# Performance work log

Measured on AMD Instinct MI355X. Metric: run time of the kernel, lower is better.

The kernel has to match this reference:

```python
import jax, jax.numpy as jnp
import numpy as np

# Static problem dims (match input_specs)
B, N, C, H, W = 1, 3, 128, 256, 256
HEADS = 4
# _compute_dynamic_scales(256,256) with max_attention_size=4096:
# min_scale = max(2, int(sqrt(65536/4096))) = 4 -> scales [4,8,16], sorted desc:
SCALES = [16, 8, 4]


def setup_inputs() -> dict:
    key = jax.random.key(0)
    ks = jax.random.split(key, 8)
    S = len(SCALES)
    std = 0.05  # small init to keep logits in a sane range
    return {
        "query": jax.random.normal(ks[0], (B, C, H, W), jnp.float32),
        "keys": jax.random.normal(ks[1], (B, N, C, H, W), jnp.float32),
        "values": jax.random.normal(ks[2], (B, N, C, H, W), jnp.float32),
        "wq": jax.random.normal(ks[3], (S, C, C), jnp.float32) * std,
        "bq": jnp.zeros((S, C), jnp.float32),
        "wk": jax.random.normal(ks[4], (S, C, C), jnp.float32) * std,
        "bk": jnp.zeros((S, C), jnp.float32),
        "wv": jax.random.normal(ks[5], (S, C, C), jnp.float32) * std,
        "bv": jnp.zeros((S, C), jnp.float32),
        "fusion_w": jax.random.normal(ks[6], (C, 3 * C), jnp.float32) * std,
        "fusion_b": jnp.zeros((C,), jnp.float32),
        "out_w": jax.random.normal(ks[7], (C, C), jnp.float32) * std,
        "out_b": jnp.zeros((C,), jnp.float32),
    }


def _pool(x, s):
    """Average pool by integer factor s over the last two dims (adaptive_avg_pool2d
    with divisible sizes)."""
    *lead, c, h, w = x.shape
    return x.reshape(*lead, c, h // s, s, w // s, s).mean(axis=(-3, -1))


def _conv1x1(x, w, b):
    # x: [..., C_in, H, W], w: [C_out, C_in], b: [C_out]
    y = jnp.einsum('...chw,oc->...ohw', x, w)
    return y + b.reshape((1,) * (y.ndim - 3) + (-1, 1, 1))


def reference(query, keys, values, wq, bq, wk, bk, wv, bv,
              fusion_w, fusion_b, out_w, out_b):
    hd = C // HEADS
    outs = []
    for si, s in enumerate(SCALES):
        Hs, Ws = H // s, W // s
        L = Hs * Ws
        q_s = _pool(query, s)   # [B,C,Hs,Ws]
        k_s = _pool(keys, s)    # [B,N,C,Hs,Ws]
        v_s = _pool(values, s)  # [B,N,C,Hs,Ws]
        q = _conv1x1(q_s, wq[si], bq[si])
        k = _conv1x1(k_s, wk[si], bk[si])
        v = _conv1x1(v_s, wv[si], bv[si])
        q = q.reshape(B, HEADS, hd, L).transpose(0, 1, 3, 2)       # [B,h,L,d]
        k = k.reshape(B, N, HEADS, hd, L)                          # [B,N,h,d,M]
        v = v.reshape(B, N, HEADS, hd, L).transpose(0, 1, 2, 4, 3) # [B,N,h,M,d]
        scores = jnp.einsum('bhld,bnhdm->bnhlm', q, k) * (hd ** -0.5)
        attn = jax.nn.softmax(scores, axis=-1)                      # stable softmax
        out = jnp.einsum('bnhlm,bnhmd->bnhld', attn, v).mean(axis=1)  # mean over anchors
        out = out.transpose(0, 1, 3, 2).reshape(B, C, Hs, Ws)
        if s > 1:
            # F.interpolate bilinear, align_corners=False (half-pixel centers)
            out = jax.image.resize(out, (B, C, H, W), method='bilinear')
        outs.append(out)
    fused = jnp.concatenate(outs, axis=1)  # [B, 3C, H, W]
    y = _conv1x1(fused, fusion_w, fusion_b)
    return _conv1x1(y, out_w, out_b)
```

## Files before the change

### kernel.cpp

```cpp
#include <hip/hip_runtime.h>
#include <hip/hip_bf16.h>


typedef __attribute__((ext_vector_type(8))) short bf16x8;
typedef __attribute__((ext_vector_type(4))) float f32x4;

__device__ inline ushort rne_bf16(float x) {
  uint u = __float_as_uint(x);
  return (ushort)((u + 0x7fffu + ((u >> 16) & 1u)) >> 16);
}

__device__ inline uint pk2_bf16(float a, float b) {
  float2 f2; f2.x = a; f2.y = b;
  __hip_bfloat162 h = __float22bfloat162_rn(f2);
  union { __hip_bfloat162 h; uint u; } cvt; cvt.h = h;
  return cvt.u;
}

__global__ __launch_bounds__(256) void pool4_kernel(
    const float* __restrict__ query, const float* __restrict__ keys,
    const float* __restrict__ values, float* __restrict__ out)
{
  int idx = blockIdx.x * 256 + threadIdx.x;
  int x = idx & 63, y = (idx >> 6) & 63, mc = idx >> 12;
  int map = mc >> 7, c = mc & 127;
  const float* src;
  if (map == 0)      src = query  + (size_t)c * 65536;
  else if (map <= 3) src = keys   + (size_t)((map - 1) * 128 + c) * 65536;
  else               src = values + (size_t)((map - 4) * 128 + c) * 65536;
  src += (y * 4) * 256 + x * 4;
  float s = 0.f;
#pragma unroll
  for (int r = 0; r < 4; ++r) {
    float4 v = *(const float4*)(src + r * 256);
    s += v.x + v.y + v.z + v.w;
  }
  out[idx] = s * 0.0625f;
}

__global__ __launch_bounds__(256) void pool2_kernel(
    const float* __restrict__ in, float* __restrict__ out, int hw)
{
  int idx = blockIdx.x * 256 + threadIdx.x;
  int x = idx % hw; int y = (idx / hw) % hw; int mc = idx / (hw * hw);
  int w2 = hw * 2;
  const float* s = in + (size_t)mc * w2 * w2 + (2 * y) * w2 + 2 * x;
  float2 a = *(const float2*)s;
  float2 b = *(const float2*)(s + w2);
  out[idx] = (a.x + a.y + b.x + b.y) * 0.25f;
}

__global__ __launch_bounds__(256) void precomp_kernel(
    const float* __restrict__ fusion_w, const float* __restrict__ fusion_b,
    const float* __restrict__ out_w, const float* __restrict__ out_b,
    float* __restrict__ Wc, float* __restrict__ bc)
{
  int idx = blockIdx.x * 256 + threadIdx.x;
  if (idx < 128 * 384) {
    int o = idx / 384, k = idx % 384;
    float s = 0.f;
    for (int c = 0; c < 128; ++c)
      s = fmaf(out_w[o * 128 + c], fusion_w[c * 384 + k], s);
    Wc[idx] = s;
  } else if (idx < 128 * 384 + 128) {
    int o = idx - 128 * 384;
    float s = out_b[o];
    for (int c = 0; c < 128; ++c)
      s = fmaf(out_w[o * 128 + c], fusion_b[c], s);
    bc[o] = s;
  }
}

__global__ __launch_bounds__(256) void proj_kernel(
    const float* __restrict__ pooled,
    ushort* __restrict__ qb, ushort* __restrict__ kbb, ushort* __restrict__ vbb,
    const float* __restrict__ wq, const float* __restrict__ bq,
    const float* __restrict__ wk, const float* __restrict__ bk,
    const float* __restrict__ wv, const float* __restrict__ bv,
    int si, int L, float qscale)
{
  __shared__ float Wt[32][68];
  __shared__ float Xs[32][64];
  int map = blockIdx.z;
  int o0 = blockIdx.y * 64;
  int l0 = blockIdx.x * 64;
  const float* w; const float* b; float sc = 1.f;
  if (map == 0)      { w = wq + si * 16384; b = bq + si * 128; sc = qscale; }
  else if (map <= 3) { w = wk + si * 16384; b = bk + si * 128; }
  else               { w = wv + si * 16384; b = bv + si * 128; }
  const float* src = pooled + (size_t)map * 128 * L;
  int t = threadIdx.x;
  int og = t >> 4, lg = t & 15;
  float acc[4][4] = {};
  for (int c0 = 0; c0 < 128; c0 += 32) {
    __syncthreads();
    {
      int o = t >> 2, ci = (t & 3) * 8;
      const float* wp = w + (o0 + o) * 128 + c0 + ci;
      float4 a = *(const float4*)wp, d = *(const float4*)(wp + 4);
      Wt[ci + 0][o] = a.x; Wt[ci + 1][o] = a.y; Wt[ci + 2][o] = a.z; Wt[ci + 3][o] = a.w;
      Wt[ci + 4][o] = d.x; Wt[ci + 5][o] = d.y; Wt[ci + 6][o] = d.z; Wt[ci + 7][o] = d.w;
    }
    {
      int c = t >> 3, li = (t & 7) * 8;
      const float* xp = src + (size_t)(c0 + c) * L + l0 + li;
      float4 a = *(const float4*)xp, d = *(const float4*)(xp + 4);
      *(float4*)&Xs[c][li] = a; *(float4*)&Xs[c][li + 4] = d;
    }
    __syncthreads();
#pragma unroll 8
    for (int k = 0; k < 32; ++k) {
      float4 wv4 = *(const float4*)&Wt[k][4 * og];
      float4 xv4 = *(const float4*)&Xs[k][4 * lg];
      float wa[4] = {wv4.x, wv4.y, wv4.z, wv4.w};
      float xa[4] = {xv4.x, xv4.y, xv4.z, xv4.w};
#pragma unroll
      for (int r = 0; r < 4; ++r)
#pragma unroll
        for (int c = 0; c < 4; ++c)
          acc[r][c] = fmaf(wa[r], xa[c], acc[r][c]);
    }
  }
  float4 b4 = *(const float4*)&b[o0 + 4 * og];
  float ba[4] = {b4.x, b4.y, b4.z, b4.w};
  if (map < 4) {
    ushort* dst = (map == 0) ? qb : (kbb + (size_t)(map - 1) * L * 32 * 4);
    int o4 = o0 + 4 * og;
    size_t hbase = (size_t)(o4 >> 5) * L * 32 + (o4 & 31);
#pragma unroll
    for (int li = 0; li < 4; ++li) {
      ushort4 r;
      r.x = rne_bf16((acc[0][li] + ba[0]) * sc);
      r.y = rne_bf16((acc[1][li] + ba[1]) * sc);
      r.z = rne_bf16((acc[2][li] + ba[2]) * sc);
      r.w = rne_bf16((acc[3][li] + ba[3]) * sc);
      *(ushort4*)&dst[hbase + (size_t)(l0 + 4 * lg + li) * 32] = r;
    }
  } else {
    ushort* dst = vbb + (size_t)(map - 4) * 128 * L;
    int m = l0 + 4 * lg;
#pragma unroll
    for (int oi = 0; oi < 4; ++oi) {
      int o = o0 + 4 * og + oi;
      int h = o >> 5, d = o & 31;
      ushort4 r;
      r.x = rne_bf16(acc[oi][0] + ba[oi]);
      r.y = rne_bf16(acc[oi][1] + ba[oi]);
      r.z = rne_bf16(acc[oi][2] + ba[oi]);
      r.w = rne_bf16(acc[oi][3] + ba[oi]);
      size_t off = (size_t)h * 32 * L
                 + ((size_t)(m >> 5) * 2 + (d >> 4)) * 512
                 + (size_t)(d & 15) * 32 + ((m >> 3) & 3) * 8 + (m & 7);
      *(ushort4*)&dst[off] = r;
    }
  }
}

#define PSTR 72
__global__ __launch_bounds__(256, 4) void attn_mfma_kernel(
    const ushort* __restrict__ qb, const ushort* __restrict__ kb,
    const ushort* __restrict__ vb, float* __restrict__ onp,
    float* __restrict__ lsp, int L, int msplit)
{
  __shared__ __align__(16) ushort P[2][4][16][PSTR];
  int t = threadIdx.x;
  int wave = t >> 6, lane = t & 63;
  int col = lane & 15, quad = lane >> 4;
  int head = blockIdx.y;
  int anchor = blockIdx.z / msplit, mpart = blockIdx.z % msplit;
  int l = blockIdx.x * 64 + wave * 16;
  int mlen = L / msplit, mbase = mpart * mlen;
  int ntile = mlen >> 6;

  const ushort* qh = qb + (size_t)head * L * 32;
  const ushort* kh = kb + ((size_t)anchor * 4 + head) * L * 32;
  const ushort* vh = vb + ((size_t)anchor * 4 + head) * 32 * L;

  bf16x8 qf = *(const bf16x8*)(qh + (size_t)(l + col) * 32 + quad * 8);
  const ushort* kbase = kh + (size_t)mbase * 32 + col * 32 + quad * 8;
  const ushort* vbase = vh + (size_t)(mbase >> 5) * 1024 + col * 32 + quad * 8;

  f32x4 od0 = {0.f,0.f,0.f,0.f};
  f32x4 od1 = {0.f,0.f,0.f,0.f};
  f32x4 lsa = {0.f,0.f,0.f,0.f};
  const f32x4 z = {0.f,0.f,0.f,0.f};
  const bf16x8 ones = {16256,16256,16256,16256,16256,16256,16256,16256};

  ushort* Pa = &P[0][wave][0][0];
  ushort* Pb = &P[1][wave][0][0];

  auto expstore = [&](f32x4 a0, f32x4 a1, f32x4 a2, f32x4 a3, ushort* Pw) {
    float sv[4][4] = {{a0.x,a0.y,a0.z,a0.w},{a1.x,a1.y,a1.z,a1.w},
                      {a2.x,a2.y,a2.z,a2.w},{a3.x,a3.y,a3.z,a3.w}};
#pragma unroll
    for (int j = 0; j < 4; ++j) {
      uint u0 = pk2_bf16(__builtin_amdgcn_exp2f(sv[j][0]),
                         __builtin_amdgcn_exp2f(sv[j][1]));
      uint u1 = pk2_bf16(__builtin_amdgcn_exp2f(sv[j][2]),
                         __builtin_amdgcn_exp2f(sv[j][3]));
      uint2 dw; dw.x = u0; dw.y = u1;
      *(uint2*)&Pw[col * PSTR + 16 * j + quad * 4] = dw;
    }
  };

  bf16x8 k0 = *(const bf16x8*)(kbase);
  bf16x8 k1 = *(const bf16x8*)(kbase + 512);
  bf16x8 k2 = *(const bf16x8*)(kbase + 1024);
  bf16x8 k3 = *(const bf16x8*)(kbase + 1536);
  f32x4 s0 = __builtin_amdgcn_mfma_f32_16x16x32_bf16(k0, qf, z, 0, 0, 0);
  f32x4 s1 = __builtin_amdgcn_mfma_f32_16x16x32_bf16(k1, qf, z, 0, 0, 0);
  f32x4 s2 = __builtin_amdgcn_mfma_f32_16x16x32_bf16(k2, qf, z, 0, 0, 0);
  f32x4 s3 = __builtin_amdgcn_mfma_f32_16x16x32_bf16(k3, qf, z, 0, 0, 0);
  {
    const ushort* kp1 = kbase + ((ntile > 1) ? 64 * 32 : 0);
    k0 = *(const bf16x8*)(kp1);
    k1 = *(const bf16x8*)(kp1 + 512);
    k2 = *(const bf16x8*)(kp1 + 1024);
    k3 = *(const bf16x8*)(kp1 + 1536);
  }
  expstore(s0, s1, s2, s3, Pa);

  for (int i = 1; i < ntile; ++i) {
    const ushort* kpn = kbase + ((i + 1 < ntile) ? (i + 1) * 2048 : 0);
    bf16x8 n0 = *(const bf16x8*)(kpn);
    bf16x8 n1 = *(const bf16x8*)(kpn + 512);
    bf16x8 n2 = *(const bf16x8*)(kpn + 1024);
    bf16x8 n3 = *(const bf16x8*)(kpn + 1536);
    const ushort* vpn = vbase + (i - 1) * 2048;
    bf16x8 vA = *(const bf16x8*)(vpn);
    bf16x8 vB = *(const bf16x8*)(vpn + 1024);
    bf16x8 vC = *(const bf16x8*)(vpn + 512);
    bf16x8 vD = *(const bf16x8*)(vpn + 1536);
    bf16x8 p0 = *(const bf16x8*)(&Pa[col * PSTR + quad * 8]);
    bf16x8 p1 = *(const bf16x8*)(&Pa[col * PSTR + 32 + quad * 8]);
    f32x4 t0 = __builtin_amdgcn_mfma_f32_16x16x32_bf16(k0, qf, z, 0, 0, 0);
    f32x4 t1 = __builtin_amdgcn_mfma_f32_16x16x32_bf16(k1, qf, z, 0, 0, 0);
    f32x4 t2 = __builtin_amdgcn_mfma_f32_16x16x32_bf16(k2, qf, z, 0, 0, 0);
    f32x4 t3 = __builtin_amdgcn_mfma_f32_16x16x32_bf16(k3, qf, z, 0, 0, 0);
    lsa = __builtin_amdgcn_mfma_f32_16x16x32_bf16(p0, ones, lsa, 0, 0, 0);
    lsa = __builtin_amdgcn_mfma_f32_16x16x32_bf16(p1, ones, lsa, 0, 0, 0);
    od0 = __builtin_amdgcn_mfma_f32_16x16x32_bf16(p0, vA, od0, 0, 0, 0);
    od0 = __builtin_amdgcn_mfma_f32_16x16x32_bf16(p1, vB, od0, 0, 0, 0);
    od1 = __builtin_amdgcn_mfma_f32_16x16x32_bf16(p0, vC, od1, 0, 0, 0);
    od1 = __builtin_amdgcn_mfma_f32_16x16x32_bf16(p1, vD, od1, 0, 0, 0);
    expstore(t0, t1, t2, t3, Pb);
    k0 = n0; k1 = n1; k2 = n2; k3 = n3;
    ushort* tp = Pa; Pa = Pb; Pb = tp;
  }

  {
    const ushort* vpe = vbase + (ntile - 1) * 2048;
    bf16x8 vA = *(const bf16x8*)(vpe);
    bf16x8 vB = *(const bf16x8*)(vpe + 1024);
    bf16x8 vC = *(const bf16x8*)(vpe + 512);
    bf16x8 vD = *(const bf16x8*)(vpe + 1536);
    bf16x8 p0 = *(const bf16x8*)(&Pa[col * PSTR + quad * 8]);
    bf16x8 p1 = *(const bf16x8*)(&Pa[col * PSTR + 32 + quad * 8]);
    lsa = __builtin_amdgcn_mfma_f32_16x16x32_bf16(p0, ones, lsa, 0, 0, 0);
    lsa = __builtin_amdgcn_mfma_f32_16x16x32_bf16(p1, ones, lsa, 0, 0, 0);
    od0 = __builtin_amdgcn_mfma_f32_16x16x32_bf16(p0, vA, od0, 0, 0, 0);
    od0 = __builtin_amdgcn_mfma_f32_16x16x32_bf16(p1, vB, od0, 0, 0, 0);
    od1 = __builtin_amdgcn_mfma_f32_16x16x32_bf16(p0, vC, od1, 0, 0, 0);
    od1 = __builtin_amdgcn_mfma_f32_16x16x32_bf16(p1, vD, od1, 0, 0, 0);
  }

  float* on2 = onp + ((size_t)(mpart * 3 + anchor) * 128 + (size_t)(head * 32)) * L;
  float* ls2 = lsp + ((size_t)(mpart * 3 + anchor) * 4 + head) * L;
  if (col == 0)
    *(f32x4*)&ls2[l + quad * 4] = lsa;
  *(f32x4*)&on2[(size_t)col * L + l + quad * 4]        = od0;
  *(f32x4*)&on2[(size_t)(16 + col) * L + l + quad * 4] = od1;
}

__global__ __launch_bounds__(256) void norm_kernel(
    const float* __restrict__ on4,  const float* __restrict__ ls4,  float* __restrict__ a4,
    const float* __restrict__ on8,  const float* __restrict__ ls8,  float* __restrict__ a8,
    const float* __restrict__ on16, const float* __restrict__ ls16, float* __restrict__ a16)
{
  int i = blockIdx.x * 256 + threadIdx.x;
  const float* on; const float* ls; float* ax; int L; int ms;
  if (i < 131072)      { on = on4;  ls = ls4;  ax = a4;  L = 4096; ms = 2; }
  else if (i < 163840) { i -= 131072; on = on8;  ls = ls8;  ax = a8;  L = 1024; ms = 2; }
  else                 { i -= 163840; on = on16; ls = ls16; ax = a16; L = 256; ms = 4; }
  int e = i * 4;
  int c = e / L, l = e % L;
  int h = c >> 5;
  float ax0 = 0.f, ax1 = 0.f, ax2 = 0.f, ax3 = 0.f;
  for (int a = 0; a < 3; ++a) {
    float n0 = 0.f, n1 = 0.f, n2 = 0.f, n3 = 0.f;
    float d0 = 0.f, d1 = 0.f, d2 = 0.f, d3 = 0.f;
    for (int mp = 0; mp < ms; ++mp) {
      int g = mp * 3 + a;
      float4 o = *(const float4*)&on[((size_t)g * 128 + c) * L + l];
      float4 s = *(const float4*)&ls[((size_t)g * 4 + h) * L + l];
      n0 += o.x; n1 += o.y; n2 += o.z; n3 += o.w;
      d0 += s.x; d1 += s.y; d2 += s.z; d3 += s.w;
    }
    ax0 += n0 / d0; ax1 += n1 / d1; ax2 += n2 / d2; ax3 += n3 / d3;
  }
  const float third = 1.f / 3.f;
  float4 r = make_float4(ax0 * third, ax1 * third, ax2 * third, ax3 * third);
  *(float4*)&ax[e] = r;
}

__global__ __launch_bounds__(256) void ygemm_kernel(
    const float* __restrict__ a16, const float* __restrict__ a8,
    const float* __restrict__ a4, const float* __restrict__ Wc,
    float* __restrict__ y16, float* __restrict__ y8, float* __restrict__ y4)
{
  __shared__ float Wt[32][68];
  __shared__ float Xs[32][64];
  int bx = blockIdx.x;
  int o0 = blockIdx.y * 64;
  int sci; int lt; const float* src; float* dst; int L;
  if (bx < 4)       { sci = 0; lt = bx;      src = a16; dst = y16; L = 256; }
  else if (bx < 20) { sci = 1; lt = bx - 4;  src = a8;  dst = y8;  L = 1024; }
  else              { sci = 2; lt = bx - 20; src = a4;  dst = y4;  L = 4096; }
  int l0 = lt * 64;
  int coff = sci * 128;
  int t = threadIdx.x;
  int og = t >> 4, lg = t & 15;
  float acc[4][4] = {};
  for (int c0 = 0; c0 < 128; c0 += 32) {
    __syncthreads();
    {
      int o = t >> 2, ci = (t & 3) * 8;
      const float* wp = Wc + (o0 + o) * 384 + coff + c0 + ci;
      float4 a = *(const float4*)wp, d = *(const float4*)(wp + 4);
      Wt[ci + 0][o] = a.x; Wt[ci + 1][o] = a.y; Wt[ci + 2][o] = a.z; Wt[ci + 3][o] = a.w;
      Wt[ci + 4][o] = d.x; Wt[ci + 5][o] = d.y; Wt[ci + 6][o] = d.z; Wt[ci + 7][o] = d.w;
    }
    {
      int c = t >> 3, li = (t & 7) * 8;
      const float* xp = src + (size_t)(c0 + c) * L + l0 + li;
      float4 a = *(const float4*)xp, d = *(const float4*)(xp + 4);
      *(float4*)&Xs[c][li] = a; *(float4*)&Xs[c][li + 4] = d;
    }
    __syncthreads();
#pragma unroll 8
    for (int k = 0; k < 32; ++k) {
      float4 wv4 = *(const float4*)&Wt[k][4 * og];
      float4 xv4 = *(const float4*)&Xs[k][4 * lg];
      float wa[4] = {wv4.x, wv4.y, wv4.z, wv4.w};
      float xa[4] = {xv4.x, xv4.y, xv4.z, xv4.w};
#pragma unroll
      for (int r = 0; r < 4; ++r)
#pragma unroll
        for (int c = 0; c < 4; ++c)
          acc[r][c] = fmaf(wa[r], xa[c], acc[r][c]);
    }
  }
#pragma unroll
  for (int r = 0; r < 4; ++r) {
    float4 v = make_float4(acc[r][0], acc[r][1], acc[r][2], acc[r][3]);
    *(float4*)&dst[(size_t)(o0 + 4 * og + r) * L + l0 + 4 * lg] = v;
  }
}

__device__ inline void add_bilinear(const float* __restrict__ Yrow0,
                                    const float* __restrict__ Yrow1,
                                    int ssz, float sf, float fy,
                                    int px0, float* r)
{
#pragma unroll
  for (int j = 0; j < 4; ++j) {
    float sx = (px0 + j + 0.5f) * sf - 0.5f;
    int xi = (int)floorf(sx);
    float fx = sx - xi;
    int x0 = max(xi, 0), x1 = min(xi + 1, ssz - 1);
    float a0 = Yrow0[x0], a1 = Yrow0[x1];
    float b0 = Yrow1[x0], b1 = Yrow1[x1];
    float v0 = a0 + fx * (a1 - a0);
    float v1 = b0 + fx * (b1 - b0);
    r[j] += v0 + fy * (v1 - v0);
  }
}

__global__ __launch_bounds__(256) void upsample_kernel(
    const float* __restrict__ y16, const float* __restrict__ y8,
    const float* __restrict__ y4, const float* __restrict__ bc,
    float* __restrict__ outp)
{
  int idx = blockIdx.x * 256 + threadIdx.x;
  int x4 = idx & 63, py = (idx >> 6) & 255, o = idx >> 14;
  int px0 = x4 * 4;
  float b = bc[o];
  float r[4] = {b, b, b, b};
#pragma unroll
  for (int s = 0; s < 3; ++s) {
    const float* Y; int ssz; float sf;
    if (s == 0)      { Y = y16; ssz = 16; sf = 1.f / 16.f; }
    else if (s == 1) { Y = y8;  ssz = 32; sf = 1.f / 8.f; }
    else             { Y = y4;  ssz = 64; sf = 1.f / 4.f; }
    const float* Yo = Y + (size_t)o * ssz * ssz;
    float sy = (py + 0.5f) * sf - 0.5f;
    int yi = (int)floorf(sy);
    float fy = sy - yi;
    int yy0 = max(yi, 0), yy1 = min(yi + 1, ssz - 1);
    add_bilinear(Yo + yy0 * ssz, Yo + yy1 * ssz, ssz, sf, fy, px0, r);
  }
  float4 v = make_float4(r[0], r[1], r[2], r[3]);
  *(float4*)&outp[(size_t)o * 65536 + py * 256 + px0] = v;
}

extern "C" void kernel_launch(void* const* d_in, const int* in_sizes, int n_in,
                              void* d_out, int out_size, void* d_ws, size_t ws_size,
                              hipStream_t stream) {
  const float* query    = (const float*)d_in[0];
  const float* keys     = (const float*)d_in[1];
  const float* values   = (const float*)d_in[2];
  const float* wq       = (const float*)d_in[3];
  const float* bq       = (const float*)d_in[4];
  const float* wk       = (const float*)d_in[5];
  const float* bk       = (const float*)d_in[6];
  const float* wv       = (const float*)d_in[7];
  const float* bv       = (const float*)d_in[8];
  const float* fusion_w = (const float*)d_in[9];
  const float* fusion_b = (const float*)d_in[10];
  const float* out_w    = (const float*)d_in[11];
  const float* out_b    = (const float*)d_in[12];
  float* wsf  = (float*)d_ws;
  float* outp = (float*)d_out;

  const size_t P4   = 0;
  const size_t P8   = 3670016;
  const size_t P16  = 4587520;
  const size_t ONP4  = 0;
  const size_t LSP4  = 3145728;
  const size_t ONP8  = 3244032;
  const size_t LSP8  = 4030464;
  const size_t ONP16 = 4055040;
  const size_t LSP16 = 4448256;
  const size_t Y4   = 0;
  const size_t Y8   = 524288;
  const size_t Y16  = 655360;
  const size_t QB4  = 4816896;
  const size_t KB4  = 5079040;
  const size_t VB4  = 5865472;
  const size_t QB8  = 6651904;
  const size_t KB8  = 6717440;
  const size_t VB8  = 6914048;
  const size_t QB16 = 7110656;
  const size_t KB16 = 7127040;
  const size_t VB16 = 7176192;
  const size_t A4   = 7225344;
  const size_t A8   = 7749632;
  const size_t A16  = 7880704;
  const size_t WC   = 7913472;
  const size_t BC   = 7962624;

  precomp_kernel<<<(128*384 + 128 + 255) / 256, 256, 0, stream>>>(
      fusion_w, fusion_b, out_w, out_b, wsf + WC, wsf + BC);
  pool4_kernel<<<7*128*4096/256, 256, 0, stream>>>(query, keys, values, wsf + P4);
  pool2_kernel<<<7*128*1024/256, 256, 0, stream>>>(wsf + P4, wsf + P8, 32);
  pool2_kernel<<<7*128*256/256,  256, 0, stream>>>(wsf + P8, wsf + P16, 16);

  const float qsc = 0.17677669529663687f * 1.4426950408889634f;
  proj_kernel<<<dim3(64, 2, 7), 256, 0, stream>>>(wsf + P4,
      (ushort*)(wsf + QB4), (ushort*)(wsf + KB4), (ushort*)(wsf + VB4),
      wq, bq, wk, bk, wv, bv, 2, 4096, qsc);
  proj_kernel<<<dim3(16, 2, 7), 256, 0, stream>>>(wsf + P8,
      (ushort*)(wsf + QB8), (ushort*)(wsf + KB8), (ushort*)(wsf + VB8),
      wq, bq, wk, bk, wv, bv, 1, 1024, qsc);
  proj_kernel<<<dim3(4, 2, 7), 256, 0, stream>>>(wsf + P16,
      (ushort*)(wsf + QB16), (ushort*)(wsf + KB16), (ushort*)(wsf + VB16),
      wq, bq, wk, bk, wv, bv, 0, 256, qsc);

  attn_mfma_kernel<<<dim3(64, 4, 6), 256, 0, stream>>>(
      (const ushort*)(wsf + QB4), (const ushort*)(wsf + KB4),
      (const ushort*)(wsf + VB4), wsf + ONP4, wsf + LSP4, 4096, 2);
  attn_mfma_kernel<<<dim3(16, 4, 6), 256, 0, stream>>>(
      (const ushort*)(wsf + QB8), (const ushort*)(wsf + KB8),
      (const ushort*)(wsf + VB8), wsf + ONP8, wsf + LSP8, 1024, 2);
  attn_mfma_kernel<<<dim3(4, 4, 12), 256, 0, stream>>>(
      (const ushort*)(wsf + QB16), (const ushort*)(wsf + KB16),
      (const ushort*)(wsf + VB16), wsf + ONP16, wsf + LSP16, 256, 4);

  norm_kernel<<<672, 256, 0, stream>>>(
      wsf + ONP4, wsf + LSP4, wsf + A4,
      wsf + ONP8, wsf + LSP8, wsf + A8,
      wsf + ONP16, wsf + LSP16, wsf + A16);

  ygemm_kernel<<<dim3(84, 2), 256, 0, stream>>>(
      wsf + A16, wsf + A8, wsf + A4, wsf + WC,
      wsf + Y16, wsf + Y8, wsf + Y4);
  upsample_kernel<<<8192, 256, 0, stream>>>(
      wsf + Y16, wsf + Y8, wsf + Y4, wsf + BC, outp);
}
```

Measured before the change: 459.2 us.

## Process two query tiles per wave to reuse K/V fragments in attention

Each wave now handles 32 query rows (two 16-row tiles) instead of 16, so every loaded K and V fragment feeds twice as many MFMAs. This halves global K/V traffic per query and halves the attention grid size. The scale-16 launch drops from a 4-way to a 2-way key split, which lets the normalisation kernel use a fixed, unrolled 2-way reduction. In exchange the kernel holds more accumulators and uses twice the LDS, which may lower occupancy, and the smaller grids give fewer blocks to spread across the GPU.

```diff
diff --git a/kernel.cpp b/kernel.cpp
--- a/kernel.cpp
+++ b/kernel.cpp
@@ -162,13 +162,13 @@
     const ushort* __restrict__ vb, float* __restrict__ onp,
     float* __restrict__ lsp, int L, int msplit)
 {
-  __shared__ __align__(16) ushort P[2][4][16][PSTR];
+  __shared__ __align__(16) ushort P[2][4][2][16][PSTR];
   int t = threadIdx.x;
   int wave = t >> 6, lane = t & 63;
   int col = lane & 15, quad = lane >> 4;
   int head = blockIdx.y;
   int anchor = blockIdx.z / msplit, mpart = blockIdx.z % msplit;
-  int l = blockIdx.x * 64 + wave * 16;
+  int l = blockIdx.x * 128 + wave * 32;
   int mlen = L / msplit, mbase = mpart * mlen;
   int ntile = mlen >> 6;
 
@@ -176,18 +176,20 @@
   const ushort* kh = kb + ((size_t)anchor * 4 + head) * L * 32;
   const ushort* vh = vb + ((size_t)anchor * 4 + head) * 32 * L;
 
-  bf16x8 qf = *(const bf16x8*)(qh + (size_t)(l + col) * 32 + quad * 8);
+  bf16x8 qfA = *(const bf16x8*)(qh + (size_t)(l + col) * 32 + quad * 8);
+  bf16x8 qfB = *(const bf16x8*)(qh + (size_t)(l + 16 + col) * 32 + quad * 8);
   const ushort* kbase = kh + (size_t)mbase * 32 + col * 32 + quad * 8;
   const ushort* vbase = vh + (size_t)(mbase >> 5) * 1024 + col * 32 + quad * 8;
 
-  f32x4 od0 = {0.f,0.f,0.f,0.f};
-  f32x4 od1 = {0.f,0.f,0.f,0.f};
-  f32x4 lsa = {0.f,0.f,0.f,0.f};
+  f32x4 odA0 = {0.f,0.f,0.f,0.f}, odA1 = {0.f,0.f,0.f,0.f};
+  f32x4 odB0 = {0.f,0.f,0.f,0.f}, odB1 = {0.f,0.f,0.f,0.f};
+  f32x4 lsaA = {0.f,0.f,0.f,0.f}, lsaB = {0.f,0.f,0.f,0.f};
   const f32x4 z = {0.f,0.f,0.f,0.f};
   const bf16x8 ones = {16256,16256,16256,16256,16256,16256,16256,16256};
 
-  ushort* Pa = &P[0][wave][0][0];
-  ushort* Pb = &P[1][wave][0][0];
+  ushort* Pa = &P[0][wave][0][0][0];
+  ushort* Pb = &P[1][wave][0][0][0];
+  const int HOF = 16 * PSTR;
 
   auto expstore = [&](f32x4 a0, f32x4 a1, f32x4 a2, f32x4 a3, ushort* Pw) {
     float sv[4][4] = {{a0.x,a0.y,a0.z,a0.w},{a1.x,a1.y,a1.z,a1.w},
@@ -207,44 +209,63 @@
   bf16x8 k1 = *(const bf16x8*)(kbase + 512);
   bf16x8 k2 = *(const bf16x8*)(kbase + 1024);
   bf16x8 k3 = *(const bf16x8*)(kbase + 1536);
-  f32x4 s0 = __builtin_amdgcn_mfma_f32_16x16x32_bf16(k0, qf, z, 0, 0, 0);
-  f32x4 s1 = __builtin_amdgcn_mfma_f32_16x16x32_bf16(k1, qf, z, 0, 0, 0);
-  f32x4 s2 = __builtin_amdgcn_mfma_f32_16x16x32_bf16(k2, qf, z, 0, 0, 0);
-  f32x4 s3 = __builtin_amdgcn_mfma_f32_16x16x32_bf16(k3, qf, z, 0, 0, 0);
   {
+    f32x4 t0 = __builtin_amdgcn_mfma_f32_16x16x32_bf16(k0, qfA, z, 0, 0, 0);
+    f32x4 t1 = __builtin_amdgcn_mfma_f32_16x16x32_bf16(k1, qfA, z, 0, 0, 0);
+    f32x4 t2 = __builtin_amdgcn_mfma_f32_16x16x32_bf16(k2, qfA, z, 0, 0, 0);
+    f32x4 t3 = __builtin_amdgcn_mfma_f32_16x16x32_bf16(k3, qfA, z, 0, 0, 0);
+    expstore(t0, t1, t2, t3, Pa);
+    t0 = __builtin_amdgcn_mfma_f32_16x16x32_bf16(k0, qfB, z, 0, 0, 0);
+    t1 = __builtin_amdgcn_mfma_f32_16x16x32_bf16(k1, qfB, z, 0, 0, 0);
+    t2 = __builtin_amdgcn_mfma_f32_16x16x32_bf16(k2, qfB, z, 0, 0, 0);
+    t3 = __builtin_amdgcn_mfma_f32_16x16x32_bf16(k3, qfB, z, 0, 0, 0);
     const ushort* kp1 = kbase + ((ntile > 1) ? 64 * 32 : 0);
     k0 = *(const bf16x8*)(kp1);
     k1 = *(const bf16x8*)(kp1 + 512);
     k2 = *(const bf16x8*)(kp1 + 1024);
     k3 = *(const bf16x8*)(kp1 + 1536);
-  }
-  expstore(s0, s1, s2, s3, Pa);
+    expstore(t0, t1, t2, t3, Pa + HOF);
+  }
 
   for (int i = 1; i < ntile; ++i) {
-    const ushort* kpn = kbase + ((i + 1 < ntile) ? (i + 1) * 2048 : 0);
-    bf16x8 n0 = *(const bf16x8*)(kpn);
-    bf16x8 n1 = *(const bf16x8*)(kpn + 512);
-    bf16x8 n2 = *(const bf16x8*)(kpn + 1024);
-    bf16x8 n3 = *(const bf16x8*)(kpn + 1536);
     const ushort* vpn = vbase + (i - 1) * 2048;
     bf16x8 vA = *(const bf16x8*)(vpn);
     bf16x8 vB = *(const bf16x8*)(vpn + 1024);
     bf16x8 vC = *(const bf16x8*)(vpn + 512);
     bf16x8 vD = *(const bf16x8*)(vpn + 1536);
-    bf16x8 p0 = *(const bf16x8*)(&Pa[col * PSTR + quad * 8]);
-    bf16x8 p1 = *(const bf16x8*)(&Pa[col * PSTR + 32 + quad * 8]);
-    f32x4 t0 = __builtin_amdgcn_mfma_f32_16x16x32_bf16(k0, qf, z, 0, 0, 0);
-    f32x4 t1 = __builtin_amdgcn_mfma_f32_16x16x32_bf16(k1, qf, z, 0, 0, 0);
-    f32x4 t2 = __builtin_amdgcn_mfma_f32_16x16x32_bf16(k2, qf, z, 0, 0, 0);
-    f32x4 t3 = __builtin_amdgcn_mfma_f32_16x16x32_bf16(k3, qf, z, 0, 0, 0);
-    lsa = __builtin_amdgcn_mfma_f32_16x16x32_bf16(p0, ones, lsa, 0, 0, 0);
-    lsa = __builtin_amdgcn_mfma_f32_16x16x32_bf16(p1, ones, lsa, 0, 0, 0);
-    od0 = __builtin_amdgcn_mfma_f32_16x16x32_bf16(p0, vA, od0, 0, 0, 0);
-    od0 = __builtin_amdgcn_mfma_f32_16x16x32_bf16(p1, vB, od0, 0, 0, 0);
-    od1 = __builtin_amdgcn_mfma_f32_16x16x32_bf16(p0, vC, od1, 0, 0, 0);
-    od1 = __builtin_amdgcn_mfma_f32_16x16x32_bf16(p1, vD, od1, 0, 0, 0);
+    bf16x8 pA0 = *(const bf16x8*)(&Pa[col * PSTR + quad * 8]);
+    bf16x8 pA1 = *(const bf16x8*)(&Pa[col * PSTR + 32 + quad * 8]);
+    bf16x8 pB0 = *(const bf16x8*)(&Pa[HOF + col * PSTR + quad * 8]);
+    bf16x8 pB1 = *(const bf16x8*)(&Pa[HOF + col * PSTR + 32 + quad * 8]);
+    f32x4 t0 = __builtin_amdgcn_mfma_f32_16x16x32_bf16(k0, qfA, z, 0, 0, 0);
+    f32x4 t1 = __builtin_amdgcn_mfma_f32_16x16x32_bf16(k1, qfA, z, 0, 0, 0);
+    f32x4 t2 = __builtin_amdgcn_mfma_f32_16x16x32_bf16(k2, qfA, z, 0, 0, 0);
+    f32x4 t3 = __builtin_amdgcn_mfma_f32_16x16x32_bf16(k3, qfA, z, 0, 0, 0);
+    lsaA = __builtin_amdgcn_mfma_f32_16x16x32_bf16(pA0, ones, lsaA, 0, 0, 0);
+    lsaA = __builtin_amdgcn_mfma_f32_16x16x32_bf16(pA1, ones, lsaA, 0, 0, 0);
+    odA0 = __builtin_amdgcn_mfma_f32_16x16x32_bf16(pA0, vA, odA0, 0, 0, 0);
+    odA0 = __builtin_amdgcn_mfma_f32_16x16x32_bf16(pA1, vB, odA0, 0, 0, 0);
+    odA1 = __builtin_amdgcn_mfma_f32_16x16x32_bf16(pA0, vC, odA1, 0, 0, 0);
+    odA1 = __builtin_amdgcn_mfma_f32_16x16x32_bf16(pA1, vD, odA1, 0, 0, 0);
     expstore(t0, t1, t2, t3, Pb);
-    k0 = n0; k1 = n1; k2 = n2; k3 = n3;
+    t0 = __builtin_amdgcn_mfma_f32_16x16x32_bf16(k0, qfB, z, 0, 0, 0);
+    t1 = __builtin_amdgcn_mfma_f32_16x16x32_bf16(k1, qfB, z, 0, 0, 0);
+    t2 = __builtin_amdgcn_mfma_f32_16x16x32_bf16(k2, qfB, z, 0, 0, 0);
+    t3 = __builtin_amdgcn_mfma_f32_16x16x32_bf16(k3, qfB, z, 0, 0, 0);
+    {
+      const ushort* kpn = kbase + ((i + 1 < ntile) ? (i + 1) * 2048 : 0);
+      k0 = *(const bf16x8*)(kpn);
+      k1 = *(const bf16x8*)(kpn + 512);
+      k2 = *(const bf16x8*)(kpn + 1024);
+      k3 = *(const bf16x8*)(kpn + 1536);
+    }
+    lsaB = __builtin_amdgcn_mfma_f32_16x16x32_bf16(pB0, ones, lsaB, 0, 0, 0);
+    lsaB = __builtin_amdgcn_mfma_f32_16x16x32_bf16(pB1, ones, lsaB, 0, 0, 0);
+    odB0 = __builtin_amdgcn_mfma_f32_16x16x32_bf16(pB0, vA, odB0, 0, 0, 0);
+    odB0 = __builtin_amdgcn_mfma_f32_16x16x32_bf16(pB1, vB, odB0, 0, 0, 0);
+    odB1 = __builtin_amdgcn_mfma_f32_16x16x32_bf16(pB0, vC, odB1, 0, 0, 0);
+    odB1 = __builtin_amdgcn_mfma_f32_16x16x32_bf16(pB1, vD, odB1, 0, 0, 0);
+    expstore(t0, t1, t2, t3, Pb + HOF);
     ushort* tp = Pa; Pa = Pb; Pb = tp;
   }
 
@@ -254,22 +275,34 @@
     bf16x8 vB = *(const bf16x8*)(vpe + 1024);
     bf16x8 vC = *(const bf16x8*)(vpe + 512);
     bf16x8 vD = *(const bf16x8*)(vpe + 1536);
-    bf16x8 p0 = *(const bf16x8*)(&Pa[col * PSTR + quad * 8]);
-    bf16x8 p1 = *(const bf16x8*)(&Pa[col * PSTR + 32 + quad * 8]);
-    lsa = __builtin_amdgcn_mfma_f32_16x16x32_bf16(p0, ones, lsa, 0, 0, 0);
-    lsa = __builtin_amdgcn_mfma_f32_16x16x32_bf16(p1, ones, lsa, 0, 0, 0);
-    od0 = __builtin_amdgcn_mfma_f32_16x16x32_bf16(p0, vA, od0, 0, 0, 0);
-    od0 = __builtin_amdgcn_mfma_f32_16x16x32_bf16(p1, vB, od0, 0, 0, 0);
-    od1 = __builtin_amdgcn_mfma_f32_16x16x32_bf16(p0, vC, od1, 0, 0, 0);
-    od1 = __builtin_amdgcn_mfma_f32_16x16x32_bf16(p1, vD, od1, 0, 0, 0);
+    bf16x8 pA0 = *(const bf16x8*)(&Pa[col * PSTR + quad * 8]);
+    bf16x8 pA1 = *(const bf16x8*)(&Pa[col * PSTR + 32 + quad * 8]);
+    bf16x8 pB0 = *(const bf16x8*)(&Pa[HOF + col * PSTR + quad * 8]);
+    bf16x8 pB1 = *(const bf16x8*)(&Pa[HOF + col * PSTR + 32 + quad * 8]);
+    lsaA = __builtin_amdgcn_mfma_f32_16x16x32_bf16(pA0, ones, lsaA, 0, 0, 0);
+    lsaA = __builtin_amdgcn_mfma_f32_16x16x32_bf16(pA1, ones, lsaA, 0, 0, 0);
+    odA0 = __builtin_amdgcn_mfma_f32_16x16x32_bf16(pA0, vA, odA0, 0, 0, 0);
+    odA0 = __builtin_amdgcn_mfma_f32_16x16x32_bf16(pA1, vB, odA0, 0, 0, 0);
+    odA1 = __builtin_amdgcn_mfma_f32_16x16x32_bf16(pA0, vC, odA1, 0, 0, 0);
+    odA1 = __builtin_amdgcn_mfma_f32_16x16x32_bf16(pA1, vD, odA1, 0, 0, 0);
+    lsaB = __builtin_amdgcn_mfma_f32_16x16x32_bf16(pB0, ones, lsaB, 0, 0, 0);
+    lsaB = __builtin_amdgcn_mfma_f32_16x16x32_bf16(pB1, ones, lsaB, 0, 0, 0);
+    odB0 = __builtin_amdgcn_mfma_f32_16x16x32_bf16(pB0, vA, odB0, 0, 0, 0);
+    odB0 = __builtin_amdgcn_mfma_f32_16x16x32_bf16(pB1, vB, odB0, 0, 0, 0);
+    odB1 = __builtin_amdgcn_mfma_f32_16x16x32_bf16(pB0, vC, odB1, 0, 0, 0);
+    odB1 = __builtin_amdgcn_mfma_f32_16x16x32_bf16(pB1, vD, odB1, 0, 0, 0);
   }
 
   float* on2 = onp + ((size_t)(mpart * 3 + anchor) * 128 + (size_t)(head * 32)) * L;
   float* ls2 = lsp + ((size_t)(mpart * 3 + anchor) * 4 + head) * L;
-  if (col == 0)
-    *(f32x4*)&ls2[l + quad * 4] = lsa;
-  *(f32x4*)&on2[(size_t)col * L + l + quad * 4]        = od0;
-  *(f32x4*)&on2[(size_t)(16 + col) * L + l + quad * 4] = od1;
+  if (col == 0) {
+    *(f32x4*)&ls2[l + quad * 4] = lsaA;
+    *(f32x4*)&ls2[l + 16 + quad * 4] = lsaB;
+  }
+  *(f32x4*)&on2[(size_t)col * L + l + quad * 4]             = odA0;
+  *(f32x4*)&on2[(size_t)(16 + col) * L + l + quad * 4]      = odA1;
+  *(f32x4*)&on2[(size_t)col * L + l + 16 + quad * 4]        = odB0;
+  *(f32x4*)&on2[(size_t)(16 + col) * L + l + 16 + quad * 4] = odB1;
 }
 
 __global__ __launch_bounds__(256) void norm_kernel(
@@ -278,10 +311,10 @@
     const float* __restrict__ on16, const float* __restrict__ ls16, float* __restrict__ a16)
 {
   int i = blockIdx.x * 256 + threadIdx.x;
-  const float* on; const float* ls; float* ax; int L; int ms;
-  if (i < 131072)      { on = on4;  ls = ls4;  ax = a4;  L = 4096; ms = 2; }
-  else if (i < 163840) { i -= 131072; on = on8;  ls = ls8;  ax = a8;  L = 1024; ms = 2; }
-  else                 { i -= 163840; on = on16; ls = ls16; ax = a16; L = 256; ms = 4; }
+  const float* on; const float* ls; float* ax; int L;
+  if (i < 131072)      { on = on4;  ls = ls4;  ax = a4;  L = 4096; }
+  else if (i < 163840) { i -= 131072; on = on8;  ls = ls8;  ax = a8;  L = 1024; }
+  else                 { i -= 163840; on = on16; ls = ls16; ax = a16; L = 256; }
   int e = i * 4;
   int c = e / L, l = e % L;
   int h = c >> 5;
@@ -289,7 +322,8 @@
   for (int a = 0; a < 3; ++a) {
     float n0 = 0.f, n1 = 0.f, n2 = 0.f, n3 = 0.f;
     float d0 = 0.f, d1 = 0.f, d2 = 0.f, d3 = 0.f;
-    for (int mp = 0; mp < ms; ++mp) {
+#pragma unroll
+    for (int mp = 0; mp < 2; ++mp) {
       int g = mp * 3 + a;
       float4 o = *(const float4*)&on[((size_t)g * 128 + c) * L + l];
       float4 s = *(const float4*)&ls[((size_t)g * 4 + h) * L + l];
@@ -466,15 +500,15 @@
       (ushort*)(wsf + QB16), (ushort*)(wsf + KB16), (ushort*)(wsf + VB16),
       wq, bq, wk, bk, wv, bv, 0, 256, qsc);
 
-  attn_mfma_kernel<<<dim3(64, 4, 6), 256, 0, stream>>>(
+  attn_mfma_kernel<<<dim3(32, 4, 6), 256, 0, stream>>>(
       (const ushort*)(wsf + QB4), (const ushort*)(wsf + KB4),
       (const ushort*)(wsf + VB4), wsf + ONP4, wsf + LSP4, 4096, 2);
-  attn_mfma_kernel<<<dim3(16, 4, 6), 256, 0, stream>>>(
+  attn_mfma_kernel<<<dim3(8, 4, 6), 256, 0, stream>>>(
       (const ushort*)(wsf + QB8), (const ushort*)(wsf + KB8),
       (const ushort*)(wsf + VB8), wsf + ONP8, wsf + LSP8, 1024, 2);
-  attn_mfma_kernel<<<dim3(4, 4, 12), 256, 0, stream>>>(
+  attn_mfma_kernel<<<dim3(2, 4, 6), 256, 0, stream>>>(
       (const ushort*)(wsf + QB16), (const ushort*)(wsf + KB16),
-      (const ushort*)(wsf + VB16), wsf + ONP16, wsf + LSP16, 256, 4);
+      (const ushort*)(wsf + VB16), wsf + ONP16, wsf + LSP16, 256, 2);
 
   norm_kernel<<<672, 256, 0, stream>>>(
       wsf + ONP4, wsf + LSP4, wsf + A4,
```

Measured after the change: 414.1 us. 1.11x faster.
